# Kernel optimization log

Measured on AMD Instinct MI355X. Metric: run time of the kernel, lower is better.

The kernel has to match this reference:

```python
import jax, jax.numpy as jnp
import numpy as np

S, B, H, A, FIN = 16, 512, 1024, 2513, 2048  # seq_len, batch, hidden, act_classes, feat_in


def setup_inputs() -> dict:
    key = jax.random.key(0)
    ks = jax.random.split(key, 13)
    k = 1.0 / np.sqrt(H)
    u = lambda kk, shape: jax.random.uniform(kk, shape, jnp.float32, -k, k)
    return {
        "inputs": jax.random.normal(ks[0], (S, B, FIN), jnp.float32),
        "W1": u(ks[1], (H, FIN)), "b1": u(ks[2], (H,)),
        "Wih_r": u(ks[3], (4 * H, 2 * H)), "Whh_r": u(ks[4], (4 * H, H)),
        "bih_r": u(ks[5], (4 * H,)), "bhh_r": u(ks[6], (4 * H,)),
        "Wih_u": u(ks[7], (4 * H, 2 * H)), "Whh_u": u(ks[8], (4 * H, H)),
        "bih_u": u(ks[9], (4 * H,)), "bhh_u": u(ks[10], (4 * H,)),
        "Wc": u(ks[11], (A, H)), "bc": u(ks[12], (A,)),
    }


def _lstm_cell(gates, c):
    # PyTorch gate order: input, forget, cell(g), output
    i, f, g, o = jnp.split(gates, 4, axis=-1)
    c_new = jax.nn.sigmoid(f) * c + jax.nn.sigmoid(i) * jnp.tanh(g)
    h_new = jax.nn.sigmoid(o) * jnp.tanh(c_new)
    return h_new, c_new


def reference(inputs, W1, b1, Wih_r, Whh_r, bih_r, bhh_r,
              Wih_u, Whh_u, bih_u, bhh_u, Wc, bc):
    # fc1 + duplicate-concat (dropout = identity in eval mode)
    x = inputs @ W1.T + b1                      # [S,B,H]
    x2 = jnp.concatenate([x, x], axis=-1)       # [S,B,2H]

    # --- rolling LSTM (OpenLSTM): scan, collecting h and c at every step ---
    xg_r = jnp.einsum('sbf,gf->sbg', x2, Wih_r) + bih_r  # input gate pre-acts

    def roll_step(carry, xg):
        h, c = carry
        h, c = _lstm_cell(xg + h @ Whh_r.T + bhh_r, c)
        return (h, c), (h, c)

    z = jnp.zeros((B, H), x.dtype)
    _, (hs, cs) = jax.lax.scan(roll_step, (z, z), xg_r)  # each [S,B,H]

    # --- unrolling LSTM: for each t, feed x2[t] repeated (S-t+1) times ---
    # input is constant across steps -> precompute gate contribution once
    xg_u = jnp.einsum('sbf,gf->sbg', x2, Wih_u) + bih_u + bhh_u  # [S,B,4H]

    def unroll(xg_t, h0, c0):
        def step(carry, _):
            h, c = carry
            h, c = _lstm_cell(xg_t + h @ Whh_u.T, c)
            return (h, c), h
        _, hseq = jax.lax.scan(step, (h0, c0), None, length=S + 1)
        return hseq  # [S+1,B,H]

    hall = jax.vmap(unroll)(xg_u, hs, cs)                 # [S,S+1,B,H]
    # original takes h after (S-t+1) steps -> index S-t (0-based)
    h_n = hall[jnp.arange(S), S - jnp.arange(S)]          # [S,B,H]

    preds = jnp.transpose(h_n, (1, 0, 2))                 # [B,S,H]
    y = preds @ Wc.T + bc                                 # [B,S,A]
    return y[:, -1, :]                                    # [B,A]
```

## Files before the change

### kernel.cpp

```cpp
#include <hip/hip_runtime.h>
#include <stdint.h>


typedef __attribute__((ext_vector_type(8))) short short8;
typedef __attribute__((ext_vector_type(4))) float f32x4;

#define SEQ   16
#define BATCH 512
#define HID   1024
#define GATE4 4096
#define FEAT  2048
#define ACTN  2513
#define ACTP  2560
#define SB    (SEQ * BATCH)

#define VMCNT0 asm volatile("s_waitcnt vmcnt(0)" ::: "memory")
#define BAR    __builtin_amdgcn_s_barrier()
#define SCHED0 __builtin_amdgcn_sched_barrier(0)

__device__ __forceinline__ unsigned short f2bf(float x) {
    unsigned u = __float_as_uint(x);
    u = u + 0x7FFFu + ((u >> 16) & 1u);
    return (unsigned short)(u >> 16);
}
__device__ __forceinline__ float bf2f(unsigned short h) {
    return __uint_as_float(((unsigned)h) << 16);
}
__device__ __forceinline__ float sigm(float x) { return 1.f / (1.f + __expf(-x)); }

__device__ __forceinline__ int gate_unperm(int nn) {
    return (((nn >> 4) & 3) << 10) | ((nn >> 6) << 4) | (nn & 15);
}

__device__ __forceinline__ void gload_lds16(const void* g, void* l) {
    __builtin_amdgcn_global_load_lds(
        (const __attribute__((address_space(1))) void*)g,
        (__attribute__((address_space(3))) void*)l,
        16, 0, 0);
}

template<bool OUT_BF16, bool HAS_BIAS, bool GUARD>
__global__ __launch_bounds__(256)
void gemm_bt(const unsigned short* __restrict__ A,
             const unsigned short* __restrict__ W,
             void* __restrict__ Cv,
             const float* __restrict__ bias,
             int M, int N, int K, int ldc, int nvalid)
{
    __shared__ __align__(16) unsigned short sA[2][128 * 64];
    __shared__ __align__(16) unsigned short sB[2][128 * 64];

    const int t    = threadIdx.x;
    const int lane = t & 63;
    const int wave = t >> 6;
    const int m0   = blockIdx.y * 128;
    const int n0   = blockIdx.x * 128;
    const int srow = t >> 3;
    const int schk = t & 7;
    const int swc  = (schk ^ (srow & 7)) * 8;
    const int sdst = srow * 64 + schk * 8;
    const int wm   = (wave >> 1) * 64;
    const int wn   = (wave & 1) * 64;
    const int fl   = lane & 15;
    const int fk8  = (lane >> 4) * 8;
    const int l7   = lane & 7;

    f32x4 acc[4][4] = {};

    const unsigned short* Abase = A + (size_t)(m0 + srow) * K + swc;
    const unsigned short* Wbase = W + (size_t)(n0 + srow) * K + swc;

    const int nkt = K >> 6;

#define G_STAGE(kt, buf)                                                     \
    {                                                                        \
        _Pragma("unroll")                                                    \
        for (int j = 0; j < 4; ++j) {                                        \
            gload_lds16(Abase + (size_t)j * 32 * K + (kt) * 64,              \
                        &sA[buf][sdst + j * 32 * 64]);                       \
            gload_lds16(Wbase + (size_t)j * 32 * K + (kt) * 64,              \
                        &sB[buf][sdst + j * 32 * 64]);                       \
        }                                                                    \
    }

    G_STAGE(0, 0);
    VMCNT0; BAR; SCHED0;

    int cur = 0;
    for (int kt = 0; kt < nkt; ++kt) {
        if (kt + 1 < nkt) G_STAGE(kt + 1, cur ^ 1);
        const unsigned short* sa = sA[cur];
        const unsigned short* sb = sB[cur];
#pragma unroll
        for (int kk = 0; kk < 64; kk += 32) {
            const int cs = (((kk + fk8) >> 3) ^ l7) * 8;
            short8 af[4], bfrag[4];
#pragma unroll
            for (int i = 0; i < 4; ++i)
                af[i] = *(const short8*)&sa[(wm + i * 16 + fl) * 64 + cs];
#pragma unroll
            for (int i = 0; i < 4; ++i)
                bfrag[i] = *(const short8*)&sb[(wn + i * 16 + fl) * 64 + cs];
#pragma unroll
            for (int mi = 0; mi < 4; ++mi)
#pragma unroll
                for (int ni = 0; ni < 4; ++ni)
                    acc[mi][ni] = __builtin_amdgcn_mfma_f32_16x16x32_bf16(
                        af[mi], bfrag[ni], acc[mi][ni], 0, 0, 0);
        }
        VMCNT0; BAR; SCHED0;
        cur ^= 1;
    }
#undef G_STAGE

    const int crb = (lane >> 4) * 4;
#pragma unroll
    for (int mi = 0; mi < 4; ++mi) {
#pragma unroll
        for (int ni = 0; ni < 4; ++ni) {
            const int col = n0 + wn + ni * 16 + fl;
            if (GUARD && col >= nvalid) continue;
            const float bv = HAS_BIAS ? bias[col] : 0.0f;
#pragma unroll
            for (int r = 0; r < 4; ++r) {
                const int row = m0 + wm + mi * 16 + crb + r;
                float v = acc[mi][ni][r] + bv;
                if (OUT_BF16)
                    ((unsigned short*)Cv)[(size_t)row * ldc + col] = f2bf(v);
                else
                    ((float*)Cv)[(size_t)row * ldc + col] = v;
            }
        }
    }
}

template<bool HAS_BIAS>
__global__ __launch_bounds__(256)
void lstm_step_fused(const unsigned short* __restrict__ hin,
                     const unsigned short* __restrict__ W,
                     const unsigned short* __restrict__ xg,
                     const float* __restrict__ bias,
                     float* __restrict__ c,
                     unsigned short* __restrict__ hout)
{
    __shared__ __align__(16) unsigned short sA[2][64 * 64];
    __shared__ __align__(16) unsigned short sB[2][64 * 64];

    const int t    = threadIdx.x;
    const int lane = t & 63;
    const int wave = t >> 6;
    const int m0   = blockIdx.y * 64;
    const int n0   = blockIdx.x * 64;
    const int srow = t >> 3;
    const int schk = t & 7;
    const int swc  = (schk ^ (srow & 7)) * 8;
    const int sdst = srow * 64 + schk * 8;
    const int wm   = wave * 16;
    const int fl   = lane & 15;
    const int fk8  = (lane >> 4) * 8;
    const int l7   = lane & 7;

    f32x4 acc[4] = {};

    const unsigned short* Abase = hin + (size_t)(m0 + srow) * HID + swc;
    const unsigned short* Wbase = W + (size_t)(n0 + srow) * HID + swc;

#define S_STAGE(kt, buf)                                                     \
    {                                                                        \
        _Pragma("unroll")                                                    \
        for (int j = 0; j < 2; ++j) {                                        \
            gload_lds16(Abase + (size_t)j * 32 * HID + (kt) * 64,            \
                        &sA[buf][sdst + j * 32 * 64]);                       \
            gload_lds16(Wbase + (size_t)j * 32 * HID + (kt) * 64,            \
                        &sB[buf][sdst + j * 32 * 64]);                       \
        }                                                                    \
    }

    S_STAGE(0, 0);
    VMCNT0; BAR; SCHED0;

    int cur = 0;
    for (int kt = 0; kt < 16; ++kt) {
        if (kt + 1 < 16) S_STAGE(kt + 1, cur ^ 1);
        const unsigned short* sa = sA[cur];
        const unsigned short* sb = sB[cur];
#pragma unroll
        for (int kk = 0; kk < 64; kk += 32) {
            const int cs = (((kk + fk8) >> 3) ^ l7) * 8;
            short8 af = *(const short8*)&sa[(wm + fl) * 64 + cs];
#pragma unroll
            for (int ni = 0; ni < 4; ++ni) {
                short8 bfr = *(const short8*)&sb[(ni * 16 + fl) * 64 + cs];
                acc[ni] = __builtin_amdgcn_mfma_f32_16x16x32_bf16(af, bfr, acc[ni], 0, 0, 0);
            }
        }
        VMCNT0; BAR; SCHED0;
        cur ^= 1;
    }
#undef S_STAGE

    const int crb = (lane >> 4) * 4;
    const int jj  = (n0 >> 6) * 16 + fl;
    float bv[4] = {0.f, 0.f, 0.f, 0.f};
    if (HAS_BIAS) {
#pragma unroll
        for (int ni = 0; ni < 4; ++ni) bv[ni] = bias[n0 + ni * 16 + fl];
    }
#pragma unroll
    for (int r = 0; r < 4; ++r) {
        const int b = m0 + wm + crb + r;
        float v[4];
#pragma unroll
        for (int ni = 0; ni < 4; ++ni)
            v[ni] = acc[ni][r] + bv[ni] + bf2f(xg[(size_t)b * GATE4 + n0 + ni * 16 + fl]);
        const int ci = b * HID + jj;
        float cv = sigm(v[1]) * c[ci] + sigm(v[0]) * tanhf(v[2]);
        c[ci] = cv;
        hout[ci] = f2bf(sigm(v[3]) * tanhf(cv));
    }
}

__global__ void lstm_cell0_k(const unsigned short* __restrict__ xg,
                             const float* __restrict__ bias,
                             float* __restrict__ c, unsigned short* __restrict__ h)
{
    int idx = blockIdx.x * blockDim.x + threadIdx.x;
    int b = idx >> 10, j = idx & 1023;
    int base = (j & 15) | ((j >> 4) << 6);
    float v[4];
#pragma unroll
    for (int g = 0; g < 4; ++g) {
        int col = base | (g << 4);
        v[g] = bf2f(xg[(size_t)b * GATE4 + col]) + bias[col];
    }
    float cv = sigm(v[0]) * tanhf(v[2]);
    c[idx] = cv;
    h[idx] = f2bf(sigm(v[3]) * tanhf(cv));
}

#define PB_IN   16384
#define PB_W1   (PB_IN + 2048)
#define PB_WR   (PB_W1 + 4096)
#define PB_WU   (PB_WR + 4096)
#define PB_WHR  (PB_WU + 4096)
#define PB_WHU  (PB_WHR + 4096)
#define PB_WC   (PB_WHU + 2560)
#define PB_END  (PB_WC + 26)

__device__ __forceinline__ void cvt4(const float* src, unsigned short* dst) {
    float4 v = *(const float4*)src;
    ushort4 o;
    o.x = f2bf(v.x); o.y = f2bf(v.y); o.z = f2bf(v.z); o.w = f2bf(v.w);
    *(ushort4*)dst = o;
}

__global__ void prep_all_k(const float* __restrict__ inputs, const float* __restrict__ W1,
                           const float* __restrict__ Wih_r, const float* __restrict__ Wih_u,
                           const float* __restrict__ Whh_r, const float* __restrict__ Whh_u,
                           const float* __restrict__ Wc,
                           const float* __restrict__ bih_r, const float* __restrict__ bhh_r,
                           const float* __restrict__ bih_u, const float* __restrict__ bhh_u,
                           const float* __restrict__ bc,
                           unsigned short* __restrict__ in_bf, unsigned short* __restrict__ W1b,
                           unsigned short* __restrict__ Wrb, unsigned short* __restrict__ Wub,
                           unsigned short* __restrict__ Whhrb, unsigned short* __restrict__ Whhub,
                           unsigned short* __restrict__ Wcb,
                           float* __restrict__ bihr_p, float* __restrict__ bhhr_p,
                           float* __restrict__ bu_p, float* __restrict__ bc_p)
{
    const int blk = blockIdx.x, tid = threadIdx.x;
    if (blk < PB_IN) {
        int i = blk * 256 + tid;
        cvt4(inputs + (size_t)i * 4, in_bf + (size_t)i * 4);
    } else if (blk < PB_W1) {
        int i = (blk - PB_IN) * 256 + tid;
        cvt4(W1 + (size_t)i * 4, W1b + (size_t)i * 4);
    } else if (blk < PB_WR) {
        int i = (blk - PB_W1) * 256 + tid;
        int nn = i >> 8, k4 = (i & 255) * 4;
        const float* row = Wih_r + (size_t)gate_unperm(nn) * FEAT;
        float4 a = *(const float4*)(row + k4);
        float4 b = *(const float4*)(row + HID + k4);
        ushort4 o;
        o.x = f2bf(a.x + b.x); o.y = f2bf(a.y + b.y);
        o.z = f2bf(a.z + b.z); o.w = f2bf(a.w + b.w);
        *(ushort4*)(Wrb + (size_t)nn * HID + k4) = o;
    } else if (blk < PB_WU) {
        int i = (blk - PB_WR) * 256 + tid;
        int nn = i >> 8, k4 = (i & 255) * 4;
        const float* row = Wih_u + (size_t)gate_unperm(nn) * FEAT;
        float4 a = *(const float4*)(row + k4);
        float4 b = *(const float4*)(row + HID + k4);
        ushort4 o;
        o.x = f2bf(a.x + b.x); o.y = f2bf(a.y + b.y);
        o.z = f2bf(a.z + b.z); o.w = f2bf(a.w + b.w);
        *(ushort4*)(Wub + (size_t)nn * HID + k4) = o;
    } else if (blk < PB_WHR) {
        int i = (blk - PB_WU) * 256 + tid;
        int nn = i >> 8, k4 = (i & 255) * 4;
        cvt4(Whh_r + (size_t)gate_unperm(nn) * HID + k4, Whhrb + (size_t)nn * HID + k4);
    } else if (blk < PB_WHU) {
        int i = (blk - PB_WHR) * 256 + tid;
        int nn = i >> 8, k4 = (i & 255) * 4;
        cvt4(Whh_u + (size_t)gate_unperm(nn) * HID + k4, Whhub + (size_t)nn * HID + k4);
    } else if (blk < PB_WC) {
        int i = (blk - PB_WHU) * 256 + tid;
        int g = i >> 8, k4 = (i & 255) * 4;
        if (g < ACTN) {
            cvt4(Wc + (size_t)g * HID + k4, Wcb + (size_t)g * HID + k4);
        } else {
            ushort4 o; o.x = o.y = o.z = o.w = 0;
            *(ushort4*)(Wcb + (size_t)g * HID + k4) = o;
        }
    } else {
        int i = (blk - PB_WC) * 256 + tid;
        if (i < GATE4) {
            int src = gate_unperm(i);
            bihr_p[i] = bih_r[src];
            bhhr_p[i] = bhh_r[src];
            bu_p[i]   = bih_u[src] + bhh_u[src];
        } else if (i < GATE4 + ACTP) {
            int j = i - GATE4;
            bc_p[j] = (j < ACTN) ? bc[j] : 0.f;
        }
    }
}

#define OFF_IN_BF 0ull
#define OFF_X_BF  33554432ull
#define OFF_XGR   50331648ull
#define OFF_W1    117440512ull
#define OFF_WR    121634816ull
#define OFF_WHHR  130023424ull
#define OFF_WU    138412032ull
#define OFF_WHHU  146800640ull
#define OFF_WCB   155189248ull
#define OFF_H0    160432128ull
#define OFF_H1    161480704ull
#define OFF_BC    162529280ull
#define OFF_BU    162539520ull
#define OFF_BIHR  162555904ull
#define OFF_BHHR  162572288ull

extern "C" void kernel_launch(void* const* d_in, const int* in_sizes, int n_in,
                              void* d_out, int out_size, void* d_ws, size_t ws_size,
                              hipStream_t stream)
{
    const float* inputs = (const float*)d_in[0];
    const float* W1     = (const float*)d_in[1];
    const float* b1     = (const float*)d_in[2];
    const float* Wih_r  = (const float*)d_in[3];
    const float* Whh_r  = (const float*)d_in[4];
    const float* bih_r  = (const float*)d_in[5];
    const float* bhh_r  = (const float*)d_in[6];
    const float* Wih_u  = (const float*)d_in[7];
    const float* Whh_u  = (const float*)d_in[8];
    const float* bih_u  = (const float*)d_in[9];
    const float* bhh_u  = (const float*)d_in[10];
    const float* Wc     = (const float*)d_in[11];
    const float* bc     = (const float*)d_in[12];
    float* out = (float*)d_out;
    char* ws = (char*)d_ws;

    unsigned short* in_bf = (unsigned short*)(ws + OFF_IN_BF);
    unsigned short* x_bf  = (unsigned short*)(ws + OFF_X_BF);
    unsigned short* xg_r  = (unsigned short*)(ws + OFF_XGR);
    unsigned short* W1b   = (unsigned short*)(ws + OFF_W1);
    unsigned short* Wrb   = (unsigned short*)(ws + OFF_WR);
    unsigned short* Whhrb = (unsigned short*)(ws + OFF_WHHR);
    unsigned short* Wub   = (unsigned short*)(ws + OFF_WU);
    unsigned short* Whhub = (unsigned short*)(ws + OFF_WHHU);
    unsigned short* Wcb   = (unsigned short*)(ws + OFF_WCB);
    unsigned short* h0    = (unsigned short*)(ws + OFF_H0);
    unsigned short* h1    = (unsigned short*)(ws + OFF_H1);
    float*          bc_p  = (float*)(ws + OFF_BC);
    float*          bu_p  = (float*)(ws + OFF_BU);
    float*          bihr_p= (float*)(ws + OFF_BIHR);
    float*          bhhr_p= (float*)(ws + OFF_BHHR);
    unsigned short* xg_u  = (unsigned short*)(ws + OFF_IN_BF);
    float*          c_buf = (float*)(ws + OFF_IN_BF + 4194304ull);

    const dim3 blk(256);

    prep_all_k<<<dim3(PB_END), blk, 0, stream>>>(
        inputs, W1, Wih_r, Wih_u, Whh_r, Whh_u, Wc,
        bih_r, bhh_r, bih_u, bhh_u, bc,
        in_bf, W1b, Wrb, Wub, Whhrb, Whhub, Wcb,
        bihr_p, bhhr_p, bu_p, bc_p);

    gemm_bt<true, true, false><<<dim3(HID / 128, SB / 128), blk, 0, stream>>>(
        in_bf, W1b, x_bf, b1, SB, HID, FEAT, HID, HID);

    gemm_bt<true, true, false><<<dim3(GATE4 / 128, SB / 128), blk, 0, stream>>>(
        x_bf, Wrb, xg_r, bihr_p, SB, GATE4, HID, GATE4, GATE4);

    gemm_bt<true, true, false><<<dim3(GATE4 / 128, BATCH / 128), blk, 0, stream>>>(
        x_bf + (size_t)(SEQ - 1) * BATCH * HID, Wub, xg_u, bu_p,
        BATCH, GATE4, HID, GATE4, GATE4);

    lstm_cell0_k<<<dim3(BATCH * HID / 256), blk, 0, stream>>>(xg_r, bhhr_p, c_buf, h0);
    unsigned short* hc = h0;
    unsigned short* hn = h1;
    for (int s = 1; s < SEQ; ++s) {
        lstm_step_fused<true><<<dim3(GATE4 / 64, BATCH / 64), blk, 0, stream>>>(
            hc, Whhrb, xg_r + (size_t)s * BATCH * GATE4, bhhr_p, c_buf, hn);
        unsigned short* tmp = hc; hc = hn; hn = tmp;
    }

    for (int s = 0; s < 2; ++s) {
        lstm_step_fused<false><<<dim3(GATE4 / 64, BATCH / 64), blk, 0, stream>>>(
            hc, Whhub, xg_u, nullptr, c_buf, hn);
        unsigned short* tmp = hc; hc = hn; hn = tmp;
    }

    gemm_bt<false, true, true><<<dim3(ACTP / 128, BATCH / 128), blk, 0, stream>>>(
        hc, Wcb, out, bc_p, BATCH, ACTP, HID, ACTN, ACTN);
}
```

Baseline: 497.9 us.

## Deepen GEMM and LSTM-step pipelines to four-stage K=32 LDS buffering

Both the generic bf16 GEMM and the fused LSTM step kernel move from a two-buffer, K=64 tile loop that drained all loads (vmcnt(0)) every iteration to a four-buffer, K=32 ring. Three tiles stay in flight and the wait uses partial vmcnt counts, so global-to-LDS loads overlap more MFMA work. The LDS swizzle is changed to suit 32-element rows. The trade-off is more barriers per unit of K and less MFMA work between them, and the vmcnt thresholds must exactly match the number of loads issued per stage.

```diff
diff --git a/kernel.cpp b/kernel.cpp
--- a/kernel.cpp
+++ b/kernel.cpp
@@ -14,9 +14,9 @@
 #define ACTP  2560
 #define SB    (SEQ * BATCH)
 
-#define VMCNT0 asm volatile("s_waitcnt vmcnt(0)" ::: "memory")
 #define BAR    __builtin_amdgcn_s_barrier()
 #define SCHED0 __builtin_amdgcn_sched_barrier(0)
+#define WAITV(n) asm volatile("s_waitcnt vmcnt(" #n ")" ::: "memory")
 
 __device__ __forceinline__ unsigned short f2bf(float x) {
     unsigned u = __float_as_uint(x);
@@ -47,71 +47,73 @@
              const float* __restrict__ bias,
              int M, int N, int K, int ldc, int nvalid)
 {
-    __shared__ __align__(16) unsigned short sA[2][128 * 64];
-    __shared__ __align__(16) unsigned short sB[2][128 * 64];
+    __shared__ __align__(16) unsigned short sA[4][128 * 32];
+    __shared__ __align__(16) unsigned short sB[4][128 * 32];
 
     const int t    = threadIdx.x;
     const int lane = t & 63;
     const int wave = t >> 6;
     const int m0   = blockIdx.y * 128;
     const int n0   = blockIdx.x * 128;
-    const int srow = t >> 3;
-    const int schk = t & 7;
-    const int swc  = (schk ^ (srow & 7)) * 8;
-    const int sdst = srow * 64 + schk * 8;
+    const int srow = t >> 2;
+    const int schk = t & 3;
+    const int wswz = ((t >> 2) & 3) ^ ((t >> 4) & 3);
+    const int swc  = (schk ^ wswz) * 8;
+    const int sdst = srow * 32 + schk * 8;
     const int wm   = (wave >> 1) * 64;
     const int wn   = (wave & 1) * 64;
     const int fl   = lane & 15;
-    const int fk8  = (lane >> 4) * 8;
-    const int l7   = lane & 7;
+    const int rs   = (fl & 3) ^ ((fl >> 2) & 3);
+    const int cs   = ((lane >> 4) ^ rs) * 8;
 
     f32x4 acc[4][4] = {};
 
-    const unsigned short* Abase = A + (size_t)(m0 + srow) * K + swc;
-    const unsigned short* Wbase = W + (size_t)(n0 + srow) * K + swc;
-
-    const int nkt = K >> 6;
-
-#define G_STAGE(kt, buf)                                                     \
+    const unsigned short* Ab0 = A + (size_t)(m0 + srow) * K + swc;
+    const unsigned short* Ab1 = Ab0 + (size_t)64 * K;
+    const unsigned short* Wb0 = W + (size_t)(n0 + srow) * K + swc;
+    const unsigned short* Wb1 = Wb0 + (size_t)64 * K;
+
+    const int nkt = K >> 5;
+
+#define G_STAGE(kt)                                                          \
     {                                                                        \
+        const int _b = (kt) & 3;                                             \
+        gload_lds16(Ab0 + (size_t)(kt) * 32, &sA[_b][sdst]);                 \
+        gload_lds16(Ab1 + (size_t)(kt) * 32, &sA[_b][sdst + 64 * 32]);       \
+        gload_lds16(Wb0 + (size_t)(kt) * 32, &sB[_b][sdst]);                 \
+        gload_lds16(Wb1 + (size_t)(kt) * 32, &sB[_b][sdst + 64 * 32]);       \
+    }
+
+#define G_COMP(kt)                                                           \
+    {                                                                        \
+        const unsigned short* sa = sA[(kt) & 3];                             \
+        const unsigned short* sb = sB[(kt) & 3];                             \
+        short8 af[4], bfr[4];                                                \
         _Pragma("unroll")                                                    \
-        for (int j = 0; j < 4; ++j) {                                        \
-            gload_lds16(Abase + (size_t)j * 32 * K + (kt) * 64,              \
-                        &sA[buf][sdst + j * 32 * 64]);                       \
-            gload_lds16(Wbase + (size_t)j * 32 * K + (kt) * 64,              \
-                        &sB[buf][sdst + j * 32 * 64]);                       \
-        }                                                                    \
-    }
-
-    G_STAGE(0, 0);
-    VMCNT0; BAR; SCHED0;
-
-    int cur = 0;
-    for (int kt = 0; kt < nkt; ++kt) {
-        if (kt + 1 < nkt) G_STAGE(kt + 1, cur ^ 1);
-        const unsigned short* sa = sA[cur];
-        const unsigned short* sb = sB[cur];
-#pragma unroll
-        for (int kk = 0; kk < 64; kk += 32) {
-            const int cs = (((kk + fk8) >> 3) ^ l7) * 8;
-            short8 af[4], bfrag[4];
-#pragma unroll
-            for (int i = 0; i < 4; ++i)
-                af[i] = *(const short8*)&sa[(wm + i * 16 + fl) * 64 + cs];
-#pragma unroll
-            for (int i = 0; i < 4; ++i)
-                bfrag[i] = *(const short8*)&sb[(wn + i * 16 + fl) * 64 + cs];
-#pragma unroll
-            for (int mi = 0; mi < 4; ++mi)
-#pragma unroll
-                for (int ni = 0; ni < 4; ++ni)
-                    acc[mi][ni] = __builtin_amdgcn_mfma_f32_16x16x32_bf16(
-                        af[mi], bfrag[ni], acc[mi][ni], 0, 0, 0);
-        }
-        VMCNT0; BAR; SCHED0;
-        cur ^= 1;
-    }
+        for (int i = 0; i < 4; ++i)                                          \
+            af[i] = *(const short8*)&sa[(wm + i * 16 + fl) * 32 + cs];       \
+        _Pragma("unroll")                                                    \
+        for (int i = 0; i < 4; ++i)                                          \
+            bfr[i] = *(const short8*)&sb[(wn + i * 16 + fl) * 32 + cs];      \
+        _Pragma("unroll")                                                    \
+        for (int mi = 0; mi < 4; ++mi)                                       \
+            _Pragma("unroll")                                                \
+            for (int ni = 0; ni < 4; ++ni)                                   \
+                acc[mi][ni] = __builtin_amdgcn_mfma_f32_16x16x32_bf16(       \
+                    af[mi], bfr[ni], acc[mi][ni], 0, 0, 0);                  \
+    }
+
+    G_STAGE(0); G_STAGE(1); G_STAGE(2);
+    for (int kt = 0; kt < nkt - 3; ++kt) {
+        WAITV(8); BAR; SCHED0;
+        G_STAGE(kt + 3);
+        G_COMP(kt);
+    }
+    WAITV(8); BAR; SCHED0; G_COMP(nkt - 3);
+    WAITV(4); BAR; SCHED0; G_COMP(nkt - 2);
+    WAITV(0); BAR; SCHED0; G_COMP(nkt - 1);
 #undef G_STAGE
+#undef G_COMP
 
     const int crb = (lane >> 4) * 4;
 #pragma unroll
@@ -143,61 +145,60 @@
                      float* __restrict__ c,
                      unsigned short* __restrict__ hout)
 {
-    __shared__ __align__(16) unsigned short sA[2][64 * 64];
-    __shared__ __align__(16) unsigned short sB[2][64 * 64];
+    __shared__ __align__(16) unsigned short sA[4][64 * 32];
+    __shared__ __align__(16) unsigned short sB[4][64 * 32];
 
     const int t    = threadIdx.x;
     const int lane = t & 63;
     const int wave = t >> 6;
     const int m0   = blockIdx.y * 64;
     const int n0   = blockIdx.x * 64;
-    const int srow = t >> 3;
-    const int schk = t & 7;
-    const int swc  = (schk ^ (srow & 7)) * 8;
-    const int sdst = srow * 64 + schk * 8;
+    const int srow = t >> 2;
+    const int schk = t & 3;
+    const int wswz = ((t >> 2) & 3) ^ ((t >> 4) & 3);
+    const int swc  = (schk ^ wswz) * 8;
+    const int sdst = srow * 32 + schk * 8;
     const int wm   = wave * 16;
     const int fl   = lane & 15;
-    const int fk8  = (lane >> 4) * 8;
-    const int l7   = lane & 7;
+    const int rs   = (fl & 3) ^ ((fl >> 2) & 3);
+    const int cs   = ((lane >> 4) ^ rs) * 8;
 
     f32x4 acc[4] = {};
 
-    const unsigned short* Abase = hin + (size_t)(m0 + srow) * HID + swc;
-    const unsigned short* Wbase = W + (size_t)(n0 + srow) * HID + swc;
-
-#define S_STAGE(kt, buf)                                                     \
+    const unsigned short* Ab = hin + (size_t)(m0 + srow) * HID + swc;
+    const unsigned short* Wb = W + (size_t)(n0 + srow) * HID + swc;
+
+#define S_STAGE(kt)                                                          \
     {                                                                        \
+        const int _b = (kt) & 3;                                             \
+        gload_lds16(Ab + (size_t)(kt) * 32, &sA[_b][sdst]);                  \
+        gload_lds16(Wb + (size_t)(kt) * 32, &sB[_b][sdst]);                  \
+    }
+
+#define S_COMP(kt)                                                           \
+    {                                                                        \
+        const unsigned short* sa = sA[(kt) & 3];                             \
+        const unsigned short* sb = sB[(kt) & 3];                             \
+        short8 af = *(const short8*)&sa[(wm + fl) * 32 + cs];                \
         _Pragma("unroll")                                                    \
-        for (int j = 0; j < 2; ++j) {                                        \
-            gload_lds16(Abase + (size_t)j * 32 * HID + (kt) * 64,            \
-                        &sA[buf][sdst + j * 32 * 64]);                       \
-            gload_lds16(Wbase + (size_t)j * 32 * HID + (kt) * 64,            \
-                        &sB[buf][sdst + j * 32 * 64]);                       \
+        for (int ni = 0; ni < 4; ++ni) {                                     \
+            short8 bfr = *(const short8*)&sb[(ni * 16 + fl) * 32 + cs];      \
+            acc[ni] = __builtin_amdgcn_mfma_f32_16x16x32_bf16(               \
+                af, bfr, acc[ni], 0, 0, 0);                                  \
         }                                                                    \
     }
 
-    S_STAGE(0, 0);
-    VMCNT0; BAR; SCHED0;
-
-    int cur = 0;
-    for (int kt = 0; kt < 16; ++kt) {
-        if (kt + 1 < 16) S_STAGE(kt + 1, cur ^ 1);
-        const unsigned short* sa = sA[cur];
-        const unsigned short* sb = sB[cur];
-#pragma unroll
-        for (int kk = 0; kk < 64; kk += 32) {
-            const int cs = (((kk + fk8) >> 3) ^ l7) * 8;
-            short8 af = *(const short8*)&sa[(wm + fl) * 64 + cs];
-#pragma unroll
-            for (int ni = 0; ni < 4; ++ni) {
-                short8 bfr = *(const short8*)&sb[(ni * 16 + fl) * 64 + cs];
-                acc[ni] = __builtin_amdgcn_mfma_f32_16x16x32_bf16(af, bfr, acc[ni], 0, 0, 0);
-            }
-        }
-        VMCNT0; BAR; SCHED0;
-        cur ^= 1;
-    }
+    S_STAGE(0); S_STAGE(1); S_STAGE(2);
+    for (int kt = 0; kt < 29; ++kt) {
+        WAITV(4); BAR; SCHED0;
+        S_STAGE(kt + 3);
+        S_COMP(kt);
+    }
+    WAITV(4); BAR; SCHED0; S_COMP(29);
+    WAITV(2); BAR; SCHED0; S_COMP(30);
+    WAITV(0); BAR; SCHED0; S_COMP(31);
 #undef S_STAGE
+#undef S_COMP
 
     const int crb = (lane >> 4) * 4;
     const int jj  = (n0 >> 6) * 16 + fl;
```

After: 545.6 us. +9.6%, slower.
